# Performance work log

Hardware: AMD Instinct MI355X
Metric: run time of the kernel (lower is better)

Reference implementation:

```python
import jax, jax.numpy as jnp
import numpy as np

DIM = 768
HEADS = 12
HEAD_DIM = DIM // HEADS
SCALE = HEAD_DIM ** -0.5


def setup_inputs() -> dict:
    key = jax.random.key(0)
    ks = jax.random.split(key, 6)
    B, N = 4, 2048
    x = jax.random.normal(ks[0], (B, N, DIM), dtype=jnp.float32)
    s = DIM ** -0.5
    Wq = jax.random.normal(ks[1], (DIM, DIM), dtype=jnp.float32) * s
    Wk = jax.random.normal(ks[2], (DIM, DIM), dtype=jnp.float32) * s
    Wv = jax.random.normal(ks[3], (DIM, DIM), dtype=jnp.float32) * s
    Wp = jax.random.normal(ks[4], (DIM, DIM), dtype=jnp.float32) * s
    bp = jnp.zeros((DIM,), dtype=jnp.float32)
    return {"x": x, "Wq": Wq, "Wk": Wk, "Wv": Wv, "Wp": Wp, "bp": bp}


def reference(x, Wq, Wk, Wv, Wp, bp):
    B, N, C = x.shape
    # separate Q/K/V linears (no bias, qkv_bias=False); torch Linear: x @ W.T
    q = (x @ Wq.T).reshape(B, N, HEADS, HEAD_DIM).transpose(0, 2, 1, 3)
    k = (x @ Wk.T).reshape(B, N, HEADS, HEAD_DIM).transpose(0, 2, 1, 3)
    v = (x @ Wv.T).reshape(B, N, HEADS, HEAD_DIM).transpose(0, 2, 1, 3)
    # explicit full [B,H,N,N] attention matrix, as in the source
    attn = jnp.einsum("bhqd,bhkd->bhqk", q, k) * SCALE
    attn = jax.nn.softmax(attn, axis=-1)
    out = jnp.einsum("bhqk,bhkd->bhqd", attn, v)
    out = out.transpose(0, 2, 1, 3).reshape(B, N, C)
    return out @ Wp.T + bp
```

## Files before the change

kernel.cpp:

```cpp
#include <hip/hip_runtime.h>
#include <cstdint>

#define DIM   768
#define HEADS 12
#define HDIM  64
#define BATCH 4
#define SEQ   2048
#define MROWS (BATCH*SEQ)

typedef __bf16 bf16;
typedef __bf16 bf16x4_t __attribute__((ext_vector_type(4)));
typedef __bf16 bf16x8_t __attribute__((ext_vector_type(8)));
typedef float  f32x4_t  __attribute__((ext_vector_type(4)));
typedef float  f32x16_t __attribute__((ext_vector_type(16)));

#define X4   (MROWS * DIM / 4)
#define W4   (DIM * DIM / 4)
#define ALL4 (X4 + 4 * W4)

__global__ void cast_all_kernel(const float* __restrict__ x,
                                const float* __restrict__ w0, const float* __restrict__ w1,
                                const float* __restrict__ w2, const float* __restrict__ w3,
                                bf16* __restrict__ xd,
                                bf16* __restrict__ d0, bf16* __restrict__ d1,
                                bf16* __restrict__ d2, bf16* __restrict__ d3) {
    int i = blockIdx.x * blockDim.x + threadIdx.x;
    if (i >= ALL4) return;
    const float* src; bf16* dst; int j;
    if (i < X4) { src = x; dst = xd; j = i; }
    else {
        int t = i - X4;  int y = t / W4;  j = t - y * W4;
        src = (y == 0) ? w0 : (y == 1) ? w1 : (y == 2) ? w2 : w3;
        dst = (y == 0) ? d0 : (y == 1) ? d1 : (y == 2) ? d2 : d3;
    }
    const float4 v = reinterpret_cast<const float4*>(src)[j];
    bf16x4_t o;
    o[0] = (bf16)v.x; o[1] = (bf16)v.y; o[2] = (bf16)v.z; o[3] = (bf16)v.w;
    reinterpret_cast<bf16x4_t*>(dst)[j] = o;
}

__device__ __forceinline__ void gload_lds16(const bf16* g, bf16* l) {
    __builtin_amdgcn_global_load_lds((const __attribute__((address_space(1))) void*)g,
                                     (__attribute__((address_space(3))) void*)l, 16, 0, 0);
}

__device__ __forceinline__ int swz4(int row) { return (row & 3) ^ ((row >> 2) & 3); }

__global__ __launch_bounds__(256, 3) void qkvv_gemm(
        const bf16* __restrict__ X,
        const bf16* __restrict__ Wq, const bf16* __restrict__ Wk, const bf16* __restrict__ Wv,
        bf16* __restrict__ Q, bf16* __restrict__ Kd, bf16* __restrict__ Vt)
{
    __shared__ __align__(16) bf16 SM[2][2][128 * 32];
    const int tid  = threadIdx.x;

    const int d  = blockIdx.x + 6 * blockIdx.y + 384 * blockIdx.z;
    const int L  = (d & 7) * 144 + (d >> 3);
    const int z  = L / 384;
    const int rem = L % 384;
    const int m0 = (rem % 6) * 128;
    const int n0 = (rem / 6) * 128;

    const bf16* Ap = (z == 0) ? Wq : (z == 1 ? Wk : Wv);
    const int lane = tid & 63;
    const int w    = tid >> 6;
    const int wm   = (w & 1) * 64, wn = (w >> 1) * 64;
    const int lr   = lane & 15, quad = lane >> 4;

    const int sr1 = tid >> 2, sc1 = tid & 3;
    const int sr2 = (tid + 256) >> 2;
    const int g1 = sc1 ^ swz4(sr1);
    const int g2 = sc1 ^ swz4(sr2);

    f32x4_t acc[4][4] = {};

    {
        gload_lds16(Ap + (size_t)(m0 + sr1) * DIM + g1 * 8, &SM[0][0][tid * 8]);
        gload_lds16(X  + (size_t)(n0 + sr1) * DIM + g1 * 8, &SM[0][1][tid * 8]);
        gload_lds16(Ap + (size_t)(m0 + sr2) * DIM + g2 * 8, &SM[0][0][(tid + 256) * 8]);
        gload_lds16(X  + (size_t)(n0 + sr2) * DIM + g2 * 8, &SM[0][1][(tid + 256) * 8]);
    }
    __syncthreads();

    int buf = 0;
    for (int p = 0; p < DIM / 32; ++p) {
        if (p + 1 < DIM / 32) {
            int kk = (p + 1) * 32;
            gload_lds16(Ap + (size_t)(m0 + sr1) * DIM + kk + g1 * 8, &SM[buf ^ 1][0][tid * 8]);
            gload_lds16(X  + (size_t)(n0 + sr1) * DIM + kk + g1 * 8, &SM[buf ^ 1][1][tid * 8]);
            gload_lds16(Ap + (size_t)(m0 + sr2) * DIM + kk + g2 * 8, &SM[buf ^ 1][0][(tid + 256) * 8]);
            gload_lds16(X  + (size_t)(n0 + sr2) * DIM + kk + g2 * 8, &SM[buf ^ 1][1][(tid + 256) * 8]);
        }
        bf16x8_t af[4], bfr[4];
        #pragma unroll
        for (int i = 0; i < 4; ++i) {
            int row = wm + i * 16 + lr;
            af[i] = *reinterpret_cast<const bf16x8_t*>(&SM[buf][0][row * 32 + (quad ^ swz4(row)) * 8]);
        }
        #pragma unroll
        for (int j = 0; j < 4; ++j) {
            int row = wn + j * 16 + lr;
            bfr[j] = *reinterpret_cast<const bf16x8_t*>(&SM[buf][1][row * 32 + (quad ^ swz4(row)) * 8]);
        }
        #pragma unroll
        for (int i = 0; i < 4; ++i)
            #pragma unroll
            for (int j = 0; j < 4; ++j)
                acc[i][j] = __builtin_amdgcn_mfma_f32_16x16x32_bf16(af[i], bfr[j], acc[i][j], 0, 0, 0);
        __syncthreads();
        buf ^= 1;
    }

    if (z == 2) {
        bf16* CT = &SM[0][0][0];
        #pragma unroll
        for (int i = 0; i < 4; ++i) {
            int ml = wm + i * 16 + quad * 4;
            #pragma unroll
            for (int j = 0; j < 4; ++j) {
                int p   = lr >> 2;
                int pp  = ((p & 1) << 1) | (p >> 1);
                int nl  = wn + j * 16 + (pp << 2) + (lr & 3);
                #pragma unroll
                for (int r = 0; r < 4; ++r)
                    CT[(ml + r) * 128 + nl] = (bf16)acc[i][j][r];
            }
        }
        __syncthreads();
        const int rr = tid >> 4, cc = tid & 15;
        #pragma unroll
        for (int rnd = 0; rnd < 8; ++rnd) {
            int ml = rnd * 16 + rr;
            *reinterpret_cast<bf16x8_t*>(&Vt[(size_t)(m0 + ml) * MROWS + n0 + cc * 8]) =
                *reinterpret_cast<const bf16x8_t*>(&CT[ml * 128 + cc * 8]);
        }
    } else {
        const float sc = (z == 0) ? 0.18033688011112042f : 1.0f;
        bf16* dst = (z == 0) ? Q : Kd;
        #pragma unroll
        for (int i = 0; i < 4; ++i) {
            int mb = m0 + wm + i * 16 + quad * 4;
            int h  = mb >> 6, d0 = mb & 63;
            #pragma unroll
            for (int j = 0; j < 4; ++j) {
                int sample = n0 + wn + j * 16 + lr;
                int b = sample >> 11, srow = sample & 2047;
                bf16x4_t o;
                #pragma unroll
                for (int r = 0; r < 4; ++r)
                    o[r] = (bf16)(acc[i][j][r] * sc);
                *reinterpret_cast<bf16x4_t*>(
                    &dst[(((size_t)b * HEADS + h) * SEQ + srow) * HDIM + d0]) = o;
            }
        }
    }
}

__global__ __launch_bounds__(256, 4) void out_gemm(
        const bf16* __restrict__ A,
        const bf16* __restrict__ W,
        const float* __restrict__ bias,
        float* __restrict__ out)
{
    __shared__ __align__(16) bf16 SA[2][64 * 32];
    __shared__ __align__(16) bf16 SB[2][128 * 32];
    const int tid  = threadIdx.x;

    const int d  = blockIdx.x + 6 * blockIdx.y;
    const int L  = (d & 7) * 96 + (d >> 3);
    const int n0 = (L % 6) * 128;
    const int m0 = (L / 6) * 64;

    const int lane = tid & 63;
    const int w    = tid >> 6;
    const int wm   = (w & 1) * 32, wn = (w >> 1) * 64;
    const int lr   = lane & 15, quad = lane >> 4;

    const int sr1 = tid >> 2, sc1 = tid & 3;
    const int sr2 = (tid + 256) >> 2;
    const int g1 = sc1 ^ swz4(sr1);
    const int g2 = sc1 ^ swz4(sr2);

    f32x4_t acc[2][4] = {};

    {
        gload_lds16(A + (size_t)(m0 + sr1) * DIM + g1 * 8, &SA[0][tid * 8]);
        gload_lds16(W + (size_t)(n0 + sr1) * DIM + g1 * 8, &SB[0][tid * 8]);
        gload_lds16(W + (size_t)(n0 + sr2) * DIM + g2 * 8, &SB[0][(tid + 256) * 8]);
    }
    __syncthreads();

    int buf = 0;
    for (int p = 0; p < DIM / 32; ++p) {
        if (p + 1 < DIM / 32) {
            int kk = (p + 1) * 32;
            gload_lds16(A + (size_t)(m0 + sr1) * DIM + kk + g1 * 8, &SA[buf ^ 1][tid * 8]);
            gload_lds16(W + (size_t)(n0 + sr1) * DIM + kk + g1 * 8, &SB[buf ^ 1][tid * 8]);
            gload_lds16(W + (size_t)(n0 + sr2) * DIM + kk + g2 * 8, &SB[buf ^ 1][(tid + 256) * 8]);
        }
        bf16x8_t af[2], bfr[4];
        #pragma unroll
        for (int i = 0; i < 2; ++i) {
            int row = wm + i * 16 + lr;
            af[i] = *reinterpret_cast<const bf16x8_t*>(&SA[buf][row * 32 + (quad ^ swz4(row)) * 8]);
        }
        #pragma unroll
        for (int j = 0; j < 4; ++j) {
            int row = wn + j * 16 + lr;
            bfr[j] = *reinterpret_cast<const bf16x8_t*>(&SB[buf][row * 32 + (quad ^ swz4(row)) * 8]);
        }
        #pragma unroll
        for (int i = 0; i < 2; ++i)
            #pragma unroll
            for (int j = 0; j < 4; ++j)
                acc[i][j] = __builtin_amdgcn_mfma_f32_16x16x32_bf16(af[i], bfr[j], acc[i][j], 0, 0, 0);
        __syncthreads();
        buf ^= 1;
    }

    #pragma unroll
    for (int i = 0; i < 2; ++i) {
        int mbase = m0 + wm + i * 16 + quad * 4;
        #pragma unroll
        for (int j = 0; j < 4; ++j) {
            int n = n0 + wn + j * 16 + lr;
            float bv = bias[n];
            #pragma unroll
            for (int r = 0; r < 4; ++r) {
                int m = mbase + r;
                out[(size_t)m * DIM + n] = acc[i][j][r] + bv;
            }
        }
    }
}

__global__ __launch_bounds__(256, 3) void attn_kernel(
        const bf16* __restrict__ Q, const bf16* __restrict__ Kd,
        const bf16* __restrict__ Vt, bf16* __restrict__ Ab)
{
    __shared__ __align__(16) bf16 SH[5 * 64 * 64];
    bf16* Kb = SH;
    bf16* Vb = SH + 2 * 4096;

    const int tid  = threadIdx.x;

    const int dd = blockIdx.x + 16 * blockIdx.y;
    const int L  = (dd & 7) * 96 + (dd >> 3);
    const int bh = L >> 4;
    const int q0 = (L & 15) * 128;

    const int b    = bh / HEADS, h = bh % HEADS;
    const int lane = tid & 63, w = tid >> 6;
    const int l31  = lane & 31, hw = lane >> 5;
    const int wq   = w * 32;

    const size_t qkbase = (size_t)bh * SEQ * HDIM;
    const size_t vbase  = (size_t)h * HDIM * MROWS + (size_t)b * SEQ;

    const int src_row  = tid >> 3, src_ch = tid & 7;
    const int src_gch  = src_ch ^ (src_row & 7);
    const int src_row2 = (tid + 256) >> 3;
    const int src_gch2 = src_ch ^ (src_row2 & 7);
    const int loff1 = src_row  * 64 + src_ch * 8;
    const int loff2 = src_row2 * 64 + src_ch * 8;

    {
        bf16* Qst = Vb + 4096;
        #pragma unroll
        for (int i = 0; i < 4; ++i) {
            int c = tid + i * 256;
            int row = c >> 3, ch = c & 7;
            int gch = ch ^ (row & 7);
            gload_lds16(Q + qkbase + (size_t)(q0 + row) * HDIM + gch * 8, Qst + row * 64 + ch * 8);
        }
    }

    const bf16* kp1 = Kd + qkbase + (size_t)src_row  * HDIM + src_gch  * 8;
    const bf16* kp2 = Kd + qkbase + (size_t)src_row2 * HDIM + src_gch2 * 8;
    const bf16* vp1 = Vt + vbase  + (size_t)src_row  * MROWS + src_gch  * 8;
    const bf16* vp2 = Vt + vbase  + (size_t)src_row2 * MROWS + src_gch2 * 8;
    const ptrdiff_t kstep = 64 * HDIM, vstep = 64;

    gload_lds16(kp1, Kb + loff1); gload_lds16(kp2, Kb + loff2);
    gload_lds16(vp1, Vb + loff1); gload_lds16(vp2, Vb + loff2);
    __syncthreads();

    bf16x8_t qf[4];
    {
        const bf16* Qst = Vb + 4096;
        int row = wq + l31;
        #pragma unroll
        for (int g = 0; g < 4; ++g) {
            int ch = (2 * g + hw) ^ (row & 7);
            qf[g] = *reinterpret_cast<const bf16x8_t*>(&Qst[row * 64 + ch * 8]);
        }
    }
    __syncthreads();

    f32x16_t oacc[2] = {};
    f32x16_t rsacc  = {};
    bf16x8_t pk[4];
    bf16x8_t ones8;
    #pragma unroll
    for (int i = 0; i < 8; ++i) ones8[i] = (bf16)1.0f;

    int vprev = 2, vcur = 0, vnext = 1;
    const int NT = SEQ / 64;

    for (int it = 0; it < NT; ++it) {
        if (it + 1 < NT) {
            const ptrdiff_t g = (ptrdiff_t)(it + 1);
            bf16* kd = Kb + ((it + 1) & 1) * 4096;
            bf16* vd = Vb + vnext * 4096;
            gload_lds16(kp1 + g * kstep, kd + loff1); gload_lds16(kp2 + g * kstep, kd + loff2);
            gload_lds16(vp1 + g * vstep, vd + loff1); gload_lds16(vp2 + g * vstep, vd + loff2);
        }

        const bf16* Ks = Kb + (it & 1) * 4096;

        f32x16_t sacc[2] = {};
        __builtin_amdgcn_s_setprio(1);
        #pragma unroll
        for (int kc = 0; kc < 2; ++kc) {
            int row = kc * 32 + l31;
            #pragma unroll
            for (int g = 0; g < 4; ++g) {
                int ch = (2 * g + hw) ^ (row & 7);
                bf16x8_t af = *reinterpret_cast<const bf16x8_t*>(&Ks[row * 64 + ch * 8]);
                sacc[kc] = __builtin_amdgcn_mfma_f32_32x32x16_bf16(af, qf[g], sacc[kc], 0, 0, 0);
            }
        }

        if (it > 0) {
            const bf16* Vs = Vb + vprev * 4096;
            #pragma unroll
            for (int dc = 0; dc < 2; ++dc) {
                int row = dc * 32 + l31;
                #pragma unroll
                for (int kg = 0; kg < 4; ++kg) {
                    int myc = (2 * kg + hw) ^ (row & 7);
                    bf16x8_t bb = *reinterpret_cast<const bf16x8_t*>(&Vs[row * 64 + myc * 8]);
                    oacc[dc] = __builtin_amdgcn_mfma_f32_32x32x16_bf16(pk[kg], bb, oacc[dc], 0, 0, 0);
                }
            }
            #pragma unroll
            for (int kg = 0; kg < 4; ++kg)
                rsacc = __builtin_amdgcn_mfma_f32_32x32x16_bf16(pk[kg], ones8, rsacc, 0, 0, 0);
        }
        __builtin_amdgcn_s_setprio(0);

        #pragma unroll
        for (int kg = 0; kg < 4; ++kg) {
            #pragma unroll
            for (int j = 0; j < 8; ++j)
                pk[kg][j] = (bf16)__builtin_amdgcn_exp2f(sacc[kg >> 1][(kg & 1) * 8 + j]);
        }

        __syncthreads();
        int tmp = vprev; vprev = vcur; vcur = vnext; vnext = tmp;
    }

    {
        const bf16* Vs = Vb + vprev * 4096;
        #pragma unroll
        for (int dc = 0; dc < 2; ++dc) {
            int row = dc * 32 + l31;
            #pragma unroll
            for (int kg = 0; kg < 4; ++kg) {
                int myc = (2 * kg + hw) ^ (row & 7);
                bf16x8_t bb = *reinterpret_cast<const bf16x8_t*>(&Vs[row * 64 + myc * 8]);
                oacc[dc] = __builtin_amdgcn_mfma_f32_32x32x16_bf16(pk[kg], bb, oacc[dc], 0, 0, 0);
            }
        }
        #pragma unroll
        for (int kg = 0; kg < 4; ++kg)
            rsacc = __builtin_amdgcn_mfma_f32_32x32x16_bf16(pk[kg], ones8, rsacc, 0, 0, 0);
    }

    float inv[16];
    #pragma unroll
    for (int r = 0; r < 16; ++r)
        inv[r] = 1.0f / rsacc[r];
    #pragma unroll
    for (int dc = 0; dc < 2; ++dc) {
        int d = dc * 32 + l31;
        #pragma unroll
        for (int r = 0; r < 16; ++r) {
            int q = q0 + wq + (r & 3) + 8 * (r >> 2) + 4 * hw;
            Ab[((size_t)b * SEQ + q) * DIM + h * HDIM + d] = (bf16)(oacc[dc][r] * inv[r]);
        }
    }
}

extern "C" void kernel_launch(void* const* d_in, const int* in_sizes, int n_in,
                              void* d_out, int out_size, void* d_ws, size_t ws_size,
                              hipStream_t stream) {
    (void)in_sizes; (void)n_in; (void)out_size; (void)ws_size;
    const float* x  = (const float*)d_in[0];
    const float* Wq = (const float*)d_in[1];
    const float* Wk = (const float*)d_in[2];
    const float* Wv = (const float*)d_in[3];
    const float* Wp = (const float*)d_in[4];
    const float* bp = (const float*)d_in[5];
    float* out = (float*)d_out;

    char* ws = (char*)d_ws;
    size_t off = 0;
    auto alloc = [&](size_t bytes) {
        void* p = ws + off;
        off += (bytes + 255) & ~(size_t)255;
        return p;
    };
    const size_t big = (size_t)MROWS * DIM * sizeof(bf16);
    const size_t wsz = (size_t)DIM * DIM * sizeof(bf16);
    bf16* Xb  = (bf16*)alloc(big);
    bf16* Qb  = (bf16*)alloc(big);
    bf16* Kb  = (bf16*)alloc(big);
    bf16* Vtb = (bf16*)alloc(big);
    bf16* Wqb = (bf16*)alloc(wsz);
    bf16* Wkb = (bf16*)alloc(wsz);
    bf16* Wvb = (bf16*)alloc(wsz);
    bf16* Wpb = (bf16*)alloc(wsz);
    bf16* Ab  = Xb;

    cast_all_kernel<<<(ALL4 + 255) / 256, 256, 0, stream>>>(
        x, Wq, Wk, Wv, Wp, Xb, Wqb, Wkb, Wvb, Wpb);

    qkvv_gemm<<<dim3(DIM / 128, MROWS / 128, 3), 256, 0, stream>>>(
        Xb, Wqb, Wkb, Wvb, Qb, Kb, Vtb);

    attn_kernel<<<dim3(SEQ / 128, BATCH * HEADS), 256, 0, stream>>>(Qb, Kb, Vtb, Ab);

    out_gemm<<<dim3(DIM / 128, MROWS / 64), 256, 0, stream>>>(Ab, Wpb, bp, out);
}
```

Before: 217.1 us.

## Fuse Q/K/V projections into one block sharing the X tile

Each QKV GEMM block now computes all three projections (Q, K, V) for a 128x128 tile, loading the X tile once and reusing it across the three weight tiles. The grid drops its z dimension and is a third the size, with 48 accumulator tiles per thread and double the LDS. The goal is to cut redundant X loads and LDS traffic. The cost is higher register pressure (occupancy bound lowered from 3 to 2), fewer blocks to fill the GPU, and an extra LDS transpose pass for V at the end of every block.

```diff
diff --git a/kernel.cpp b/kernel.cpp
--- a/kernel.cpp
+++ b/kernel.cpp
@@ -46,22 +46,19 @@
 
 __device__ __forceinline__ int swz4(int row) { return (row & 3) ^ ((row >> 2) & 3); }
 
-__global__ __launch_bounds__(256, 3) void qkvv_gemm(
+__global__ __launch_bounds__(256, 2) void qkvv_gemm(
         const bf16* __restrict__ X,
         const bf16* __restrict__ Wq, const bf16* __restrict__ Wk, const bf16* __restrict__ Wv,
         bf16* __restrict__ Q, bf16* __restrict__ Kd, bf16* __restrict__ Vt)
 {
-    __shared__ __align__(16) bf16 SM[2][2][128 * 32];
+    __shared__ __align__(16) bf16 SM[2][4][128 * 32];
     const int tid  = threadIdx.x;
 
-    const int d  = blockIdx.x + 6 * blockIdx.y + 384 * blockIdx.z;
-    const int L  = (d & 7) * 144 + (d >> 3);
-    const int z  = L / 384;
-    const int rem = L % 384;
-    const int m0 = (rem % 6) * 128;
-    const int n0 = (rem / 6) * 128;
-
-    const bf16* Ap = (z == 0) ? Wq : (z == 1 ? Wk : Wv);
+    const int d  = blockIdx.x + 6 * blockIdx.y;
+    const int L  = (d & 7) * 48 + (d >> 3);
+    const int m0 = (L % 6) * 128;
+    const int n0 = (L / 6) * 128;
+
     const int lane = tid & 63;
     const int w    = tid >> 6;
     const int wm   = (w & 1) * 64, wn = (w >> 1) * 64;
@@ -72,69 +69,55 @@
     const int g1 = sc1 ^ swz4(sr1);
     const int g2 = sc1 ^ swz4(sr2);
 
-    f32x4_t acc[4][4] = {};
-
-    {
-        gload_lds16(Ap + (size_t)(m0 + sr1) * DIM + g1 * 8, &SM[0][0][tid * 8]);
-        gload_lds16(X  + (size_t)(n0 + sr1) * DIM + g1 * 8, &SM[0][1][tid * 8]);
-        gload_lds16(Ap + (size_t)(m0 + sr2) * DIM + g2 * 8, &SM[0][0][(tid + 256) * 8]);
-        gload_lds16(X  + (size_t)(n0 + sr2) * DIM + g2 * 8, &SM[0][1][(tid + 256) * 8]);
-    }
+    f32x4_t acc[3][4][4] = {};
+
+    #define STAGE(B, KK)                                                                   \
+        {   int kk_ = (KK);                                                                \
+            gload_lds16(Wq + (size_t)(m0 + sr1) * DIM + kk_ + g1 * 8, &SM[B][0][tid * 8]); \
+            gload_lds16(Wk + (size_t)(m0 + sr1) * DIM + kk_ + g1 * 8, &SM[B][1][tid * 8]); \
+            gload_lds16(Wv + (size_t)(m0 + sr1) * DIM + kk_ + g1 * 8, &SM[B][2][tid * 8]); \
+            gload_lds16(X  + (size_t)(n0 + sr1) * DIM + kk_ + g1 * 8, &SM[B][3][tid * 8]); \
+            gload_lds16(Wq + (size_t)(m0 + sr2) * DIM + kk_ + g2 * 8, &SM[B][0][(tid + 256) * 8]); \
+            gload_lds16(Wk + (size_t)(m0 + sr2) * DIM + kk_ + g2 * 8, &SM[B][1][(tid + 256) * 8]); \
+            gload_lds16(Wv + (size_t)(m0 + sr2) * DIM + kk_ + g2 * 8, &SM[B][2][(tid + 256) * 8]); \
+            gload_lds16(X  + (size_t)(n0 + sr2) * DIM + kk_ + g2 * 8, &SM[B][3][(tid + 256) * 8]); \
+        }
+
+    STAGE(0, 0);
     __syncthreads();
 
     int buf = 0;
     for (int p = 0; p < DIM / 32; ++p) {
         if (p + 1 < DIM / 32) {
-            int kk = (p + 1) * 32;
-            gload_lds16(Ap + (size_t)(m0 + sr1) * DIM + kk + g1 * 8, &SM[buf ^ 1][0][tid * 8]);
-            gload_lds16(X  + (size_t)(n0 + sr1) * DIM + kk + g1 * 8, &SM[buf ^ 1][1][tid * 8]);
-            gload_lds16(Ap + (size_t)(m0 + sr2) * DIM + kk + g2 * 8, &SM[buf ^ 1][0][(tid + 256) * 8]);
-            gload_lds16(X  + (size_t)(n0 + sr2) * DIM + kk + g2 * 8, &SM[buf ^ 1][1][(tid + 256) * 8]);
-        }
-        bf16x8_t af[4], bfr[4];
-        #pragma unroll
-        for (int i = 0; i < 4; ++i) {
-            int row = wm + i * 16 + lr;
-            af[i] = *reinterpret_cast<const bf16x8_t*>(&SM[buf][0][row * 32 + (quad ^ swz4(row)) * 8]);
-        }
+            if (buf) STAGE(0, (p + 1) * 32) else STAGE(1, (p + 1) * 32);
+        }
+        bf16x8_t bfr[4];
         #pragma unroll
         for (int j = 0; j < 4; ++j) {
             int row = wn + j * 16 + lr;
-            bfr[j] = *reinterpret_cast<const bf16x8_t*>(&SM[buf][1][row * 32 + (quad ^ swz4(row)) * 8]);
-        }
-        #pragma unroll
-        for (int i = 0; i < 4; ++i)
-            #pragma unroll
-            for (int j = 0; j < 4; ++j)
-                acc[i][j] = __builtin_amdgcn_mfma_f32_16x16x32_bf16(af[i], bfr[j], acc[i][j], 0, 0, 0);
+            bfr[j] = *reinterpret_cast<const bf16x8_t*>(&SM[buf][3][row * 32 + (quad ^ swz4(row)) * 8]);
+        }
+        #pragma unroll
+        for (int z = 0; z < 3; ++z) {
+            bf16x8_t af[4];
+            #pragma unroll
+            for (int i = 0; i < 4; ++i) {
+                int row = wm + i * 16 + lr;
+                af[i] = *reinterpret_cast<const bf16x8_t*>(&SM[buf][z][row * 32 + (quad ^ swz4(row)) * 8]);
+            }
+            #pragma unroll
+            for (int i = 0; i < 4; ++i)
+                #pragma unroll
+                for (int j = 0; j < 4; ++j)
+                    acc[z][i][j] = __builtin_amdgcn_mfma_f32_16x16x32_bf16(af[i], bfr[j], acc[z][i][j], 0, 0, 0);
+        }
         __syncthreads();
         buf ^= 1;
     }
-
-    if (z == 2) {
-        bf16* CT = &SM[0][0][0];
-        #pragma unroll
-        for (int i = 0; i < 4; ++i) {
-            int ml = wm + i * 16 + quad * 4;
-            #pragma unroll
-            for (int j = 0; j < 4; ++j) {
-                int p   = lr >> 2;
-                int pp  = ((p & 1) << 1) | (p >> 1);
-                int nl  = wn + j * 16 + (pp << 2) + (lr & 3);
-                #pragma unroll
-                for (int r = 0; r < 4; ++r)
-                    CT[(ml + r) * 128 + nl] = (bf16)acc[i][j][r];
-            }
-        }
-        __syncthreads();
-        const int rr = tid >> 4, cc = tid & 15;
-        #pragma unroll
-        for (int rnd = 0; rnd < 8; ++rnd) {
-            int ml = rnd * 16 + rr;
-            *reinterpret_cast<bf16x8_t*>(&Vt[(size_t)(m0 + ml) * MROWS + n0 + cc * 8]) =
-                *reinterpret_cast<const bf16x8_t*>(&CT[ml * 128 + cc * 8]);
-        }
-    } else {
+    #undef STAGE
+
+    #pragma unroll
+    for (int z = 0; z < 2; ++z) {
         const float sc = (z == 0) ? 0.18033688011112042f : 1.0f;
         bf16* dst = (z == 0) ? Q : Kd;
         #pragma unroll
@@ -148,10 +131,35 @@
                 bf16x4_t o;
                 #pragma unroll
                 for (int r = 0; r < 4; ++r)
-                    o[r] = (bf16)(acc[i][j][r] * sc);
+                    o[r] = (bf16)(acc[z][i][j][r] * sc);
                 *reinterpret_cast<bf16x4_t*>(
                     &dst[(((size_t)b * HEADS + h) * SEQ + srow) * HDIM + d0]) = o;
             }
+        }
+    }
+
+    {
+        bf16* CT = &SM[0][0][0];
+        #pragma unroll
+        for (int i = 0; i < 4; ++i) {
+            int ml = wm + i * 16 + quad * 4;
+            #pragma unroll
+            for (int j = 0; j < 4; ++j) {
+                int pc  = lr >> 2;
+                int pp  = ((pc & 1) << 1) | (pc >> 1);
+                int nl  = wn + j * 16 + (pp << 2) + (lr & 3);
+                #pragma unroll
+                for (int r = 0; r < 4; ++r)
+                    CT[(ml + r) * 128 + nl] = (bf16)acc[2][i][j][r];
+            }
+        }
+        __syncthreads();
+        const int rr = tid >> 4, cc = tid & 15;
+        #pragma unroll
+        for (int rnd = 0; rnd < 8; ++rnd) {
+            int ml = rnd * 16 + rr;
+            *reinterpret_cast<bf16x8_t*>(&Vt[(size_t)(m0 + ml) * MROWS + n0 + cc * 8]) =
+                *reinterpret_cast<const bf16x8_t*>(&CT[ml * 128 + cc * 8]);
         }
     }
 }
@@ -426,7 +434,7 @@
     cast_all_kernel<<<(ALL4 + 255) / 256, 256, 0, stream>>>(
         x, Wq, Wk, Wv, Wp, Xb, Wqb, Wkb, Wvb, Wpb);
 
-    qkvv_gemm<<<dim3(DIM / 128, MROWS / 128, 3), 256, 0, stream>>>(
+    qkvv_gemm<<<dim3(6, MROWS / 128), 256, 0, stream>>>(
         Xb, Wqb, Wkb, Wvb, Qb, Kb, Vtb);
 
     attn_kernel<<<dim3(SEQ / 128, BATCH * HEADS), 256, 0, stream>>>(Qb, Kb, Vtb, Ab);
```

New measurement: 215.7 us. No clear change (-0.7%).

## Triple-buffer projection GEMM LDS tiles with partial vmcnt waits and single barrier

Applied to the files above, without the earlier changes.

Both projection GEMMs (QKV and output) move from double buffering with two __syncthreads per K-step to a three-stage LDS ring. Each iteration waits only for the oldest stage with s_waitcnt vmcnt(N), issues one barrier, then prefetches two steps ahead before computing. The goal is to keep more global-to-LDS loads in flight and remove a barrier per iteration so memory latency hides behind MFMA work. The cost is 50% more shared memory per block, which may reduce occupancy at the requested launch bounds. It also relies on hand-written waitcnt counts being correct for the direct-to-LDS loads.

```diff
diff --git a/kernel.cpp b/kernel.cpp
--- a/kernel.cpp
+++ b/kernel.cpp
@@ -46,12 +46,17 @@
 
 __device__ __forceinline__ int swz4(int row) { return (row & 3) ^ ((row >> 2) & 3); }
 
+__device__ __forceinline__ void lds_drain() {
+    asm volatile("s_waitcnt lgkmcnt(0)" ::: "memory");
+    __builtin_amdgcn_sched_barrier(0);
+}
+
 __global__ __launch_bounds__(256, 3) void qkvv_gemm(
         const bf16* __restrict__ X,
         const bf16* __restrict__ Wq, const bf16* __restrict__ Wk, const bf16* __restrict__ Wv,
         bf16* __restrict__ Q, bf16* __restrict__ Kd, bf16* __restrict__ Vt)
 {
-    __shared__ __align__(16) bf16 SM[2][2][128 * 32];
+    __shared__ __align__(16) bf16 SM[3][2][128 * 32];
     const int tid  = threadIdx.x;
 
     const int d  = blockIdx.x + 6 * blockIdx.y + 384 * blockIdx.z;
@@ -74,42 +79,49 @@
 
     f32x4_t acc[4][4] = {};
 
-    {
-        gload_lds16(Ap + (size_t)(m0 + sr1) * DIM + g1 * 8, &SM[0][0][tid * 8]);
-        gload_lds16(X  + (size_t)(n0 + sr1) * DIM + g1 * 8, &SM[0][1][tid * 8]);
-        gload_lds16(Ap + (size_t)(m0 + sr2) * DIM + g2 * 8, &SM[0][0][(tid + 256) * 8]);
-        gload_lds16(X  + (size_t)(n0 + sr2) * DIM + g2 * 8, &SM[0][1][(tid + 256) * 8]);
-    }
-    __syncthreads();
-
-    int buf = 0;
-    for (int p = 0; p < DIM / 32; ++p) {
-        if (p + 1 < DIM / 32) {
-            int kk = (p + 1) * 32;
-            gload_lds16(Ap + (size_t)(m0 + sr1) * DIM + kk + g1 * 8, &SM[buf ^ 1][0][tid * 8]);
-            gload_lds16(X  + (size_t)(n0 + sr1) * DIM + kk + g1 * 8, &SM[buf ^ 1][1][tid * 8]);
-            gload_lds16(Ap + (size_t)(m0 + sr2) * DIM + kk + g2 * 8, &SM[buf ^ 1][0][(tid + 256) * 8]);
-            gload_lds16(X  + (size_t)(n0 + sr2) * DIM + kk + g2 * 8, &SM[buf ^ 1][1][(tid + 256) * 8]);
-        }
-        bf16x8_t af[4], bfr[4];
-        #pragma unroll
-        for (int i = 0; i < 4; ++i) {
-            int row = wm + i * 16 + lr;
-            af[i] = *reinterpret_cast<const bf16x8_t*>(&SM[buf][0][row * 32 + (quad ^ swz4(row)) * 8]);
-        }
-        #pragma unroll
-        for (int j = 0; j < 4; ++j) {
-            int row = wn + j * 16 + lr;
-            bfr[j] = *reinterpret_cast<const bf16x8_t*>(&SM[buf][1][row * 32 + (quad ^ swz4(row)) * 8]);
-        }
-        #pragma unroll
-        for (int i = 0; i < 4; ++i)
-            #pragma unroll
-            for (int j = 0; j < 4; ++j)
-                acc[i][j] = __builtin_amdgcn_mfma_f32_16x16x32_bf16(af[i], bfr[j], acc[i][j], 0, 0, 0);
-        __syncthreads();
-        buf ^= 1;
-    }
+    #define STAGE(B, KK)                                                                    \
+        {   int kk_ = (KK);                                                                 \
+            gload_lds16(Ap + (size_t)(m0 + sr1) * DIM + kk_ + g1 * 8, &SM[B][0][tid * 8]);  \
+            gload_lds16(X  + (size_t)(n0 + sr1) * DIM + kk_ + g1 * 8, &SM[B][1][tid * 8]);  \
+            gload_lds16(Ap + (size_t)(m0 + sr2) * DIM + kk_ + g2 * 8, &SM[B][0][(tid + 256) * 8]); \
+            gload_lds16(X  + (size_t)(n0 + sr2) * DIM + kk_ + g2 * 8, &SM[B][1][(tid + 256) * 8]); \
+        }
+
+    #define COMPUTE(B)                                                                       \
+        {   bf16x8_t af[4], bfr[4];                                                          \
+            _Pragma("unroll")                                                                \
+            for (int i = 0; i < 4; ++i) {                                                    \
+                int row = wm + i * 16 + lr;                                                  \
+                af[i] = *reinterpret_cast<const bf16x8_t*>(&SM[B][0][row * 32 + (quad ^ swz4(row)) * 8]); \
+            }                                                                                \
+            _Pragma("unroll")                                                                \
+            for (int j = 0; j < 4; ++j) {                                                    \
+                int row = wn + j * 16 + lr;                                                  \
+                bfr[j] = *reinterpret_cast<const bf16x8_t*>(&SM[B][1][row * 32 + (quad ^ swz4(row)) * 8]); \
+            }                                                                                \
+            _Pragma("unroll")                                                                \
+            for (int i = 0; i < 4; ++i)                                                      \
+                _Pragma("unroll")                                                            \
+                for (int j = 0; j < 4; ++j)                                                  \
+                    acc[i][j] = __builtin_amdgcn_mfma_f32_16x16x32_bf16(af[i], bfr[j], acc[i][j], 0, 0, 0); \
+        }
+
+    STAGE(0, 0);
+    STAGE(1, 32);
+
+    for (int p = 0; p < 23; ++p) {
+        asm volatile("s_waitcnt vmcnt(4)" ::: "memory");
+        __builtin_amdgcn_s_barrier();
+        if (p + 2 < 24) STAGE((p + 2) % 3, (p + 2) * 32);
+        COMPUTE(p % 3);
+        lds_drain();
+    }
+    asm volatile("s_waitcnt vmcnt(0)" ::: "memory");
+    __builtin_amdgcn_s_barrier();
+    COMPUTE(2);
+    lds_drain();
+    #undef STAGE
+    #undef COMPUTE
 
     if (z == 2) {
         bf16* CT = &SM[0][0][0];
@@ -118,8 +130,8 @@
             int ml = wm + i * 16 + quad * 4;
             #pragma unroll
             for (int j = 0; j < 4; ++j) {
-                int p   = lr >> 2;
-                int pp  = ((p & 1) << 1) | (p >> 1);
+                int pc  = lr >> 2;
+                int pp  = ((pc & 1) << 1) | (pc >> 1);
                 int nl  = wn + j * 16 + (pp << 2) + (lr & 3);
                 #pragma unroll
                 for (int r = 0; r < 4; ++r)
@@ -162,8 +174,8 @@
         const float* __restrict__ bias,
         float* __restrict__ out)
 {
-    __shared__ __align__(16) bf16 SA[2][64 * 32];
-    __shared__ __align__(16) bf16 SB[2][128 * 32];
+    __shared__ __align__(16) bf16 SA[3][64 * 32];
+    __shared__ __align__(16) bf16 SB[3][128 * 32];
     const int tid  = threadIdx.x;
 
     const int d  = blockIdx.x + 6 * blockIdx.y;
@@ -183,40 +195,47 @@
 
     f32x4_t acc[2][4] = {};
 
-    {
-        gload_lds16(A + (size_t)(m0 + sr1) * DIM + g1 * 8, &SA[0][tid * 8]);
-        gload_lds16(W + (size_t)(n0 + sr1) * DIM + g1 * 8, &SB[0][tid * 8]);
-        gload_lds16(W + (size_t)(n0 + sr2) * DIM + g2 * 8, &SB[0][(tid + 256) * 8]);
-    }
-    __syncthreads();
-
-    int buf = 0;
-    for (int p = 0; p < DIM / 32; ++p) {
-        if (p + 1 < DIM / 32) {
-            int kk = (p + 1) * 32;
-            gload_lds16(A + (size_t)(m0 + sr1) * DIM + kk + g1 * 8, &SA[buf ^ 1][tid * 8]);
-            gload_lds16(W + (size_t)(n0 + sr1) * DIM + kk + g1 * 8, &SB[buf ^ 1][tid * 8]);
-            gload_lds16(W + (size_t)(n0 + sr2) * DIM + kk + g2 * 8, &SB[buf ^ 1][(tid + 256) * 8]);
-        }
-        bf16x8_t af[2], bfr[4];
-        #pragma unroll
-        for (int i = 0; i < 2; ++i) {
-            int row = wm + i * 16 + lr;
-            af[i] = *reinterpret_cast<const bf16x8_t*>(&SA[buf][row * 32 + (quad ^ swz4(row)) * 8]);
-        }
-        #pragma unroll
-        for (int j = 0; j < 4; ++j) {
-            int row = wn + j * 16 + lr;
-            bfr[j] = *reinterpret_cast<const bf16x8_t*>(&SB[buf][row * 32 + (quad ^ swz4(row)) * 8]);
-        }
-        #pragma unroll
-        for (int i = 0; i < 2; ++i)
-            #pragma unroll
-            for (int j = 0; j < 4; ++j)
-                acc[i][j] = __builtin_amdgcn_mfma_f32_16x16x32_bf16(af[i], bfr[j], acc[i][j], 0, 0, 0);
-        __syncthreads();
-        buf ^= 1;
-    }
+    #define STAGE(B, KK)                                                                    \
+        {   int kk_ = (KK);                                                                 \
+            gload_lds16(A + (size_t)(m0 + sr1) * DIM + kk_ + g1 * 8, &SA[B][tid * 8]);      \
+            gload_lds16(W + (size_t)(n0 + sr1) * DIM + kk_ + g1 * 8, &SB[B][tid * 8]);      \
+            gload_lds16(W + (size_t)(n0 + sr2) * DIM + kk_ + g2 * 8, &SB[B][(tid + 256) * 8]); \
+        }
+
+    #define COMPUTE(B)                                                                       \
+        {   bf16x8_t af[2], bfr[4];                                                          \
+            _Pragma("unroll")                                                                \
+            for (int i = 0; i < 2; ++i) {                                                    \
+                int row = wm + i * 16 + lr;                                                  \
+                af[i] = *reinterpret_cast<const bf16x8_t*>(&SA[B][row * 32 + (quad ^ swz4(row)) * 8]); \
+            }                                                                                \
+            _Pragma("unroll")                                                                \
+            for (int j = 0; j < 4; ++j) {                                                    \
+                int row = wn + j * 16 + lr;                                                  \
+                bfr[j] = *reinterpret_cast<const bf16x8_t*>(&SB[B][row * 32 + (quad ^ swz4(row)) * 8]); \
+            }                                                                                \
+            _Pragma("unroll")                                                                \
+            for (int i = 0; i < 2; ++i)                                                      \
+                _Pragma("unroll")                                                            \
+                for (int j = 0; j < 4; ++j)                                                  \
+                    acc[i][j] = __builtin_amdgcn_mfma_f32_16x16x32_bf16(af[i], bfr[j], acc[i][j], 0, 0, 0); \
+        }
+
+    STAGE(0, 0);
+    STAGE(1, 32);
+
+    for (int p = 0; p < 23; ++p) {
+        asm volatile("s_waitcnt vmcnt(3)" ::: "memory");
+        __builtin_amdgcn_s_barrier();
+        if (p + 2 < 24) STAGE((p + 2) % 3, (p + 2) * 32);
+        COMPUTE(p % 3);
+        lds_drain();
+    }
+    asm volatile("s_waitcnt vmcnt(0)" ::: "memory");
+    __builtin_amdgcn_s_barrier();
+    COMPUTE(2);
+    #undef STAGE
+    #undef COMPUTE
 
     #pragma unroll
     for (int i = 0; i < 2; ++i) {
```

New measurement: 209.7 us. 3.4% less time.
